# Optimization experiments

Hardware: AMD Instinct MI355X
Metric: run time of the kernel (lower is better)

## Reference

```python
import jax, jax.numpy as jnp
import numpy as np

EPS = 1e-12  # F.normalize default eps

def _l2norm(x, axis):
    n = jnp.sqrt(jnp.sum(x * x, axis=axis, keepdims=True))
    return x / jnp.maximum(n, EPS)

def setup_inputs() -> dict:
    key = jax.random.key(0)
    ks = jax.random.split(key, 6)
    N, C, K, B, OUT = 200000, 256, 64, 8, 1024
    alpha = 100.0
    feat = jax.random.normal(ks[0], (N, C), dtype=jnp.float32)
    batch_ids = jax.random.randint(ks[1], (N,), 0, B, dtype=jnp.int32)
    centroids = jax.random.uniform(ks[2], (K, C), dtype=jnp.float32)
    # _init_params: conv weight = 2*alpha*centroids, bias = -alpha*||centroid||_2
    conv_w = 2.0 * alpha * centroids
    conv_b = -alpha * jnp.sqrt(jnp.sum(centroids * centroids, axis=1))
    fc_w = jax.random.normal(ks[3], (OUT, K * C), dtype=jnp.float32) * (1.0 / np.sqrt(K * C))
    fc_b = jax.random.normal(ks[4], (OUT,), dtype=jnp.float32) * 0.01
    return {"feat": feat, "batch_ids": batch_ids, "centroids": centroids,
            "conv_w": conv_w, "conv_b": conv_b, "fc_w": fc_w, "fc_b": fc_b,
            "batch_size": B}

def reference(feat, batch_ids, centroids, conv_w, conv_b, fc_w, fc_b, batch_size):
    B = int(batch_size)
    K, C = centroids.shape
    # descriptor-wise L2 normalization (normalize_input=True)
    x = _l2norm(feat, axis=1)                       # [N, C]
    # 1x1 conv == linear: soft assignment logits per point
    logits = x @ conv_w.T + conv_b                  # [N, K]
    soft = jax.nn.softmax(logits, axis=1)           # [N, K]
    # Per-batch aggregation (replaces the python loop):
    # vlad[b,k,:] = sum_{p in b} soft[p,k] * x[p,:] - (sum_{p in b} soft[p,k]) * centroids[k,:]
    onehot = jax.nn.one_hot(batch_ids, B, dtype=x.dtype)          # [N, B]
    A = jnp.einsum('nb,nk,nc->bkc', onehot, soft, x)              # [B, K, C]
    S = jax.ops.segment_sum(soft, batch_ids, num_segments=B)      # [B, K]
    vlad = A - S[:, :, None] * centroids[None, :, :]              # [B, K, C]
    vlad = _l2norm(vlad, axis=2)                                  # intra-normalization over C
    v = vlad.reshape(B, K * C)
    out = v @ fc_w.T + fc_b                                       # [B, 1024]
    return _l2norm(out, axis=1)
```

## Files before the change

kernel.cpp:

```cpp
#include <hip/hip_runtime.h>
#include <hip/hip_bf16.h>

typedef __attribute__((ext_vector_type(8))) short bf16x8;
typedef __attribute__((ext_vector_type(4))) float f32x4;

#define PCAP 768

__device__ __forceinline__ void async_copy16(const void* g, void* l)
{
    __builtin_amdgcn_global_load_lds(
        (const __attribute__((address_space(1))) unsigned int*)g,
        (__attribute__((address_space(3))) unsigned int*)l, 16, 0, 0);
}

__global__ void p0_wsplit(const float* __restrict__ convw,
                          short* __restrict__ whi, short* __restrict__ wlo)
{
    int e = blockIdx.x * 256 + threadIdx.x;
    if (e >= 2048) return;
    int lane = e & 63;
    int kstep = (e >> 6) & 7;
    int nt = e >> 9;
    int cluster = nt * 16 + (lane & 15);
    int ch0 = kstep * 32 + (lane >> 4) * 8;
    const float* src = convw + cluster * 256 + ch0;
    #pragma unroll
    for (int j = 0; j < 8; ++j) {
        float x = src[j];
        unsigned u = __float_as_uint(x);
        unsigned uh = u & 0xffff0000u;
        float r = x - __uint_as_float(uh);
        whi[e * 8 + j] = (short)(u >> 16);
        wlo[e * 8 + j] = (short)(__float_as_uint(r) >> 16);
    }
}

__global__ __launch_bounds__(256, 2) void p1_mfma(
    const float* __restrict__ feat, const int* __restrict__ bids,
    const short* __restrict__ whi, const short* __restrict__ wlo,
    const float* __restrict__ convb,
    float* __restrict__ soft, float* __restrict__ invn, int* __restrict__ cnts, int N)
{
    __shared__ short whL[2048 * 8];
    __shared__ short wlL[2048 * 8];
    __shared__ int cnt[8];
    const int t = threadIdx.x;
    if (t < 8) cnt[t] = 0;
    const int w = t >> 6, lane = t & 63;
    const int m = lane & 15, quad = lane >> 4;
    const int p0 = blockIdx.x * 64;
    const int gp = p0 + w * 16 + m;
    const bool valid = gp < N;

    #pragma unroll
    for (int pass = 0; pass < 8; ++pass) {
        async_copy16((const bf16x8*)whi + pass * 256 + t,
                     (char*)whL + (size_t)(pass * 256 + w * 64) * 16);
        async_copy16((const bf16x8*)wlo + pass * 256 + t,
                     (char*)wlL + (size_t)(pass * 256 + w * 64) * 16);
    }

    const float* frow = valid ? (feat + (size_t)gp * 256 + quad * 8) : feat;
    float4 xv[16];
    #pragma unroll
    for (int ks = 0; ks < 8; ++ks) {
        xv[2 * ks]     = *(const float4*)(frow + ks * 32);
        xv[2 * ks + 1] = *(const float4*)(frow + ks * 32 + 4);
    }

    __syncthreads();

    f32x4 acc[4];
    #pragma unroll
    for (int nt = 0; nt < 4; ++nt) acc[nt] = (f32x4){0.f, 0.f, 0.f, 0.f};
    float ssq = 0.f;

    #pragma unroll
    for (int ks = 0; ks < 8; ++ks) {
        float x[8] = {xv[2 * ks].x, xv[2 * ks].y, xv[2 * ks].z, xv[2 * ks].w,
                      xv[2 * ks + 1].x, xv[2 * ks + 1].y, xv[2 * ks + 1].z, xv[2 * ks + 1].w};
        bf16x8 ahi, alo;
        #pragma unroll
        for (int j = 0; j < 8; ++j) {
            unsigned u = __float_as_uint(x[j]);
            float r = x[j] - __uint_as_float(u & 0xffff0000u);
            ahi[j] = (short)(u >> 16);
            alo[j] = (short)(__float_as_uint(r) >> 16);
            ssq += x[j] * x[j];
        }
        #pragma unroll
        for (int nt = 0; nt < 4; ++nt) {
            bf16x8 bh = *(const bf16x8*)&whL[(size_t)((nt * 8 + ks) * 64 + lane) * 8];
            bf16x8 bl = *(const bf16x8*)&wlL[(size_t)((nt * 8 + ks) * 64 + lane) * 8];
            acc[nt] = __builtin_amdgcn_mfma_f32_16x16x32_bf16(ahi, bh, acc[nt], 0, 0, 0);
            acc[nt] = __builtin_amdgcn_mfma_f32_16x16x32_bf16(ahi, bl, acc[nt], 0, 0, 0);
            acc[nt] = __builtin_amdgcn_mfma_f32_16x16x32_bf16(alo, bh, acc[nt], 0, 0, 0);
        }
    }

    ssq += __shfl_xor(ssq, 16);
    ssq += __shfl_xor(ssq, 32);

    float bias[4];
    #pragma unroll
    for (int nt = 0; nt < 4; ++nt) bias[nt] = convb[nt * 16 + m];

    #pragma unroll
    for (int r = 0; r < 4; ++r) {
        int pl = quad * 4 + r;
        int gpt = p0 + w * 16 + pl;
        float sq = __shfl(ssq, pl);
        float inv = rsqrtf(fmaxf(sq, 1e-24f));
        float v[4];
        #pragma unroll
        for (int nt = 0; nt < 4; ++nt) v[nt] = acc[nt][r] * inv + bias[nt];
        float mx = fmaxf(fmaxf(v[0], v[1]), fmaxf(v[2], v[3]));
        #pragma unroll
        for (int off = 8; off >= 1; off >>= 1) mx = fmaxf(mx, __shfl_xor(mx, off));
        float e[4];
        float s = 0.f;
        #pragma unroll
        for (int nt = 0; nt < 4; ++nt) { e[nt] = __expf(v[nt] - mx); s += e[nt]; }
        #pragma unroll
        for (int off = 8; off >= 1; off >>= 1) s += __shfl_xor(s, off);
        float rs = 1.0f / s;
        if (gpt < N) {
            #pragma unroll
            for (int nt = 0; nt < 4; ++nt)
                soft[(size_t)gpt * 64 + nt * 16 + m] = e[nt] * rs;
            if (m == 0) {
                invn[gpt] = inv;
                atomicAdd(&cnt[bids[gpt]], 1);
            }
        }
    }
    __syncthreads();
    if (t < 8) atomicAdd(&cnts[t], cnt[t]);
}

__global__ void p2_offsets(const int* __restrict__ cnts, int* __restrict__ offs, int* __restrict__ cur)
{
    if (threadIdx.x == 0) {
        int acc = 0;
        for (int b = 0; b < 8; ++b) { offs[b] = acc; cur[b] = acc; acc += cnts[b]; }
        offs[8] = acc;
    }
}

__global__ __launch_bounds__(256) void p2_scatter(
    const int* __restrict__ bids, int* __restrict__ cur, int* __restrict__ perm, int N)
{
    __shared__ int lcnt[8], lbase[8];
    const int t = threadIdx.x;
    if (t < 8) lcnt[t] = 0;
    __syncthreads();
    int p = blockIdx.x * 256 + t;
    int b = 0, my = 0;
    bool ok = p < N;
    if (ok) { b = bids[p]; my = atomicAdd(&lcnt[b], 1); }
    __syncthreads();
    if (t < 8) lbase[t] = atomicAdd(&cur[t], lcnt[t]);
    __syncthreads();
    if (ok) perm[lbase[b] + my] = p;
}

__global__ __launch_bounds__(256, 2) void p3_mfma(
    const float* __restrict__ feat, const float* __restrict__ soft,
    const float* __restrict__ invn, const int* __restrict__ perm,
    const int* __restrict__ offs, float* __restrict__ partial,
    float* __restrict__ S, int split)
{
    __shared__ short xsT_hi[256 * 32];
    __shared__ short xsT_lo[256 * 32];
    __shared__ short sT_hi[64 * 32];
    __shared__ short sT_lo[64 * 32];
    __shared__ int   pidxL[PCAP];
    __shared__ float invL[PCAP];

    const int b  = blockIdx.x / split;
    const int sp = blockIdx.x % split;
    const int start = offs[b], end = offs[b + 1];
    const int len = end - start;
    const int chunk = (len + split - 1) / split;
    const int s0 = start + sp * chunk;
    int myLen = end - s0;
    myLen = max(0, min(myLen, chunk));
    myLen = min(myLen, PCAP);

    const int t = threadIdx.x;
    const int w = t >> 6, lane = t & 63;
    const int m = lane & 15, quad = lane >> 4;

    for (int i = t; i < myLen; i += 256) pidxL[i] = perm[s0 + i];
    __syncthreads();
    for (int i = t; i < myLen; i += 256) invL[i] = invn[pidxL[i]];
    __syncthreads();

    f32x4 acc[16];
    #pragma unroll
    for (int ct = 0; ct < 16; ++ct) acc[ct] = (f32x4){0.f, 0.f, 0.f, 0.f};
    float sacc = 0.f;

    const int nch = (myLen + 31) >> 5;

    int   pids[8];
    float pinv[8];
    float xv[4][8];
    float sv[8];

    auto FETCH = [&](int q) {
        const int p0 = q * 32;
        #pragma unroll
        for (int j = 0; j < 8; ++j) {
            int pl = p0 + w * 8 + j;
            bool ok = pl < myLen;
            pids[j] = ok ? pidxL[pl] : -1;
            pinv[j] = ok ? invL[pl] : 0.f;
        }
        #pragma unroll
        for (int cg = 0; cg < 4; ++cg) {
            int c = cg * 64 + lane;
            #pragma unroll
            for (int j = 0; j < 8; ++j)
                xv[cg][j] = (pids[j] >= 0) ? feat[(size_t)pids[j] * 256 + c] : 0.f;
        }
        #pragma unroll
        for (int j = 0; j < 8; ++j)
            sv[j] = (pids[j] >= 0) ? soft[(size_t)pids[j] * 64 + lane] : 0.f;
    };

    if (nch > 0) FETCH(0);

    for (int q = 0; q < nch; ++q) {
        __syncthreads();
        #pragma unroll
        for (int cg = 0; cg < 4; ++cg) {
            int c = cg * 64 + lane;
            bf16x8 vh, vl;
            #pragma unroll
            for (int j = 0; j < 8; ++j) {
                float v = xv[cg][j] * pinv[j];
                unsigned u = __float_as_uint(v);
                float r = v - __uint_as_float(u & 0xffff0000u);
                vh[j] = (short)(u >> 16);
                vl[j] = (short)(__float_as_uint(r) >> 16);
            }
            int slot = (w ^ (c & 3)) * 8;
            *(bf16x8*)&xsT_hi[c * 32 + slot] = vh;
            *(bf16x8*)&xsT_lo[c * 32 + slot] = vl;
        }
        {
            bf16x8 vh, vl;
            #pragma unroll
            for (int j = 0; j < 8; ++j) {
                float v = sv[j];
                sacc += v;
                unsigned u = __float_as_uint(v);
                float r = v - __uint_as_float(u & 0xffff0000u);
                vh[j] = (short)(u >> 16);
                vl[j] = (short)(__float_as_uint(r) >> 16);
            }
            int slot = (w ^ (lane & 3)) * 8;
            *(bf16x8*)&sT_hi[lane * 32 + slot] = vh;
            *(bf16x8*)&sT_lo[lane * 32 + slot] = vl;
        }
        if (q + 1 < nch) FETCH(q + 1);
        __syncthreads();
        {
            const int arow = w * 16 + m;
            const int aslot = (quad ^ (m & 3)) * 8;
            bf16x8 ah = *(const bf16x8*)&sT_hi[arow * 32 + aslot];
            bf16x8 al = *(const bf16x8*)&sT_lo[arow * 32 + aslot];
            const int bslot = (quad ^ (m & 3)) * 8;
            #pragma unroll
            for (int ct = 0; ct < 16; ++ct) {
                const int brow = ct * 16 + m;
                bf16x8 bh = *(const bf16x8*)&xsT_hi[brow * 32 + bslot];
                bf16x8 bl = *(const bf16x8*)&xsT_lo[brow * 32 + bslot];
                acc[ct] = __builtin_amdgcn_mfma_f32_16x16x32_bf16(ah, bh, acc[ct], 0, 0, 0);
                acc[ct] = __builtin_amdgcn_mfma_f32_16x16x32_bf16(ah, bl, acc[ct], 0, 0, 0);
                acc[ct] = __builtin_amdgcn_mfma_f32_16x16x32_bf16(al, bh, acc[ct], 0, 0, 0);
            }
        }
    }

    float* dst = partial + (size_t)(b * split + sp) * 64 * 256;
    #pragma unroll
    for (int ct = 0; ct < 16; ++ct) {
        #pragma unroll
        for (int r = 0; r < 4; ++r) {
            int k = w * 16 + quad * 4 + r;
            dst[k * 256 + ct * 16 + m] = acc[ct][r];
        }
    }
    atomicAdd(S + b * 64 + lane, sacc);
}

__global__ __launch_bounds__(256) void p4a_vlad(
    const float* __restrict__ partial, const float* __restrict__ S,
    const float* __restrict__ cents, float* __restrict__ v, int split)
{
    const int b = blockIdx.x >> 6, k = blockIdx.x & 63;
    const int t = threadIdx.x;
    float sum = 0.f;
    const float* base = partial + ((size_t)(b * split) * 64 + k) * 256 + t;
    for (int sp = 0; sp < split; ++sp)
        sum += base[(size_t)sp * 64 * 256];
    float val = sum - S[b * 64 + k] * cents[k * 256 + t];
    float sq = val * val;
    #pragma unroll
    for (int off = 32; off >= 1; off >>= 1) sq += __shfl_xor(sq, off);
    __shared__ float wsum[4];
    if ((t & 63) == 0) wsum[t >> 6] = sq;
    __syncthreads();
    float tot = wsum[0] + wsum[1] + wsum[2] + wsum[3];
    float r = 1.0f / fmaxf(sqrtf(tot), 1e-12f);
    v[b * 16384 + k * 256 + t] = val * r;
}

__global__ __launch_bounds__(256) void p4b_fc(
    const float* __restrict__ v, const float* __restrict__ fcw,
    const float* __restrict__ fcb, float* __restrict__ pre)
{
    const int t = threadIdx.x;
    const int o0 = blockIdx.x * 4;
    float acc[4][8] = {};
    for (int it = 0; it < 64; ++it) {
        int i = it * 256 + t;
        float wv[4];
        #pragma unroll
        for (int oo = 0; oo < 4; ++oo) wv[oo] = fcw[(size_t)(o0 + oo) * 16384 + i];
        #pragma unroll
        for (int b = 0; b < 8; ++b) {
            float vv = v[b * 16384 + i];
            #pragma unroll
            for (int oo = 0; oo < 4; ++oo) acc[oo][b] += wv[oo] * vv;
        }
    }
    __shared__ float red[32][4];
    #pragma unroll
    for (int oo = 0; oo < 4; ++oo)
        #pragma unroll
        for (int b = 0; b < 8; ++b) {
            float sv = acc[oo][b];
            #pragma unroll
            for (int off = 32; off >= 1; off >>= 1) sv += __shfl_xor(sv, off);
            if ((t & 63) == 0) red[oo * 8 + b][t >> 6] = sv;
        }
    __syncthreads();
    if (t < 32) {
        int oo = t >> 3, b = t & 7;
        float sv = red[t][0] + red[t][1] + red[t][2] + red[t][3];
        pre[b * 1024 + o0 + oo] = sv + fcb[o0 + oo];
    }
}

__global__ __launch_bounds__(256) void p5_norm(const float* __restrict__ pre, float* __restrict__ out)
{
    const int b = blockIdx.x, t = threadIdx.x;
    float vals[4];
    float sq = 0.f;
    #pragma unroll
    for (int i = 0; i < 4; ++i) {
        vals[i] = pre[b * 1024 + t + 256 * i];
        sq += vals[i] * vals[i];
    }
    #pragma unroll
    for (int off = 32; off >= 1; off >>= 1) sq += __shfl_xor(sq, off);
    __shared__ float wsum[4];
    if ((t & 63) == 0) wsum[t >> 6] = sq;
    __syncthreads();
    float tot = wsum[0] + wsum[1] + wsum[2] + wsum[3];
    float r = 1.0f / fmaxf(sqrtf(tot), 1e-12f);
    #pragma unroll
    for (int i = 0; i < 4; ++i) out[b * 1024 + t + 256 * i] = vals[i] * r;
}

extern "C" void kernel_launch(void* const* d_in, const int* in_sizes, int n_in,
                              void* d_out, int out_size, void* d_ws, size_t ws_size,
                              hipStream_t stream)
{
    const float* feat  = (const float*)d_in[0];
    const int*   bids  = (const int*)d_in[1];
    const float* cents = (const float*)d_in[2];
    const float* convw = (const float*)d_in[3];
    const float* convb = (const float*)d_in[4];
    const float* fcw   = (const float*)d_in[5];
    const float* fcb   = (const float*)d_in[6];
    float* out = (float*)d_out;

    const int N = in_sizes[0] / 256;

    const size_t base_floats = 16384
                             + (size_t)N * 64  + N
                             + 512  + 8 * 16384  + 8192 ;
    const size_t base_ints = (size_t)N + 8 + 9 + 8;
    int split = 96;
    while (split > 16) {
        size_t tot = (base_floats + (size_t)split * 8 * 16384) * 4 + base_ints * 4;
        if (tot <= ws_size) break;
        split -= 16;
    }

    short* whi = (short*)d_ws;
    short* wlo = whi + 16384;
    float* soft = (float*)(wlo + 16384);
    float* invn = soft + (size_t)N * 64;
    float* partial = invn + N;
    float* S    = partial + (size_t)split * 8 * 16384;
    float* v    = S + 512;
    float* pre  = v + 8 * 16384;
    int* perm = (int*)(pre + 8192);
    int* cnts = perm + N;
    int* offs = cnts + 8;
    int* cur  = offs + 9;

    hipMemsetAsync(S, 0, 512 * sizeof(float), stream);
    hipMemsetAsync(cnts, 0, 8 * sizeof(int), stream);

    p0_wsplit<<<8, 256, 0, stream>>>(convw, whi, wlo);
    p1_mfma<<<(N + 63) / 64, 256, 0, stream>>>(feat, bids, whi, wlo, convb, soft, invn, cnts, N);
    p2_offsets<<<1, 64, 0, stream>>>(cnts, offs, cur);
    p2_scatter<<<(N + 255) / 256, 256, 0, stream>>>(bids, cur, perm, N);
    p3_mfma<<<8 * split, 256, 0, stream>>>(feat, soft, invn, perm, offs, partial, S, split);
    p4a_vlad<<<512, 256, 0, stream>>>(partial, S, cents, v, split);
    p4b_fc<<<256, 256, 0, stream>>>(v, fcw, fcb, pre);
    p5_norm<<<8, 256, 0, stream>>>(pre, out);
}
```

Before: 481.0 us.

## Fuse soft-assignment logits and softmax into the per-batch aggregation kernel

Removes the separate soft-assignment kernel. The aggregation kernel now recomputes each point's L2 norm, its 64 logits via split-bf16 MFMA and the softmax for every 32-point chunk it has gathered. This drops the full-size soft and invn intermediates, their global write and read-back, and one full pass over feat. A small kernel now only counts points per batch, and S is reduced through shared memory before the atomics. In exchange the aggregation loop gets extra MFMAs, shuffles and barriers, and it reloads feature rows straight from global memory for the logit GEMM, hoping they are still cached.

```diff
diff --git a/kernel.cpp b/kernel.cpp
--- a/kernel.cpp
+++ b/kernel.cpp
@@ -5,13 +5,6 @@
 typedef __attribute__((ext_vector_type(4))) float f32x4;
 
 #define PCAP 768
-
-__device__ __forceinline__ void async_copy16(const void* g, void* l)
-{
-    __builtin_amdgcn_global_load_lds(
-        (const __attribute__((address_space(1))) unsigned int*)g,
-        (__attribute__((address_space(3))) unsigned int*)l, 16, 0, 0);
-}
 
 __global__ void p0_wsplit(const float* __restrict__ convw,
                           short* __restrict__ whi, short* __restrict__ wlo)
@@ -35,107 +28,17 @@
     }
 }
 
-__global__ __launch_bounds__(256, 2) void p1_mfma(
-    const float* __restrict__ feat, const int* __restrict__ bids,
-    const short* __restrict__ whi, const short* __restrict__ wlo,
-    const float* __restrict__ convb,
-    float* __restrict__ soft, float* __restrict__ invn, int* __restrict__ cnts, int N)
-{
-    __shared__ short whL[2048 * 8];
-    __shared__ short wlL[2048 * 8];
-    __shared__ int cnt[8];
+__global__ __launch_bounds__(256) void p2a_count(
+    const int* __restrict__ bids, int* __restrict__ cnts, int N)
+{
+    __shared__ int lcnt[8];
     const int t = threadIdx.x;
-    if (t < 8) cnt[t] = 0;
-    const int w = t >> 6, lane = t & 63;
-    const int m = lane & 15, quad = lane >> 4;
-    const int p0 = blockIdx.x * 64;
-    const int gp = p0 + w * 16 + m;
-    const bool valid = gp < N;
-
-    #pragma unroll
-    for (int pass = 0; pass < 8; ++pass) {
-        async_copy16((const bf16x8*)whi + pass * 256 + t,
-                     (char*)whL + (size_t)(pass * 256 + w * 64) * 16);
-        async_copy16((const bf16x8*)wlo + pass * 256 + t,
-                     (char*)wlL + (size_t)(pass * 256 + w * 64) * 16);
-    }
-
-    const float* frow = valid ? (feat + (size_t)gp * 256 + quad * 8) : feat;
-    float4 xv[16];
-    #pragma unroll
-    for (int ks = 0; ks < 8; ++ks) {
-        xv[2 * ks]     = *(const float4*)(frow + ks * 32);
-        xv[2 * ks + 1] = *(const float4*)(frow + ks * 32 + 4);
-    }
-
-    __syncthreads();
-
-    f32x4 acc[4];
-    #pragma unroll
-    for (int nt = 0; nt < 4; ++nt) acc[nt] = (f32x4){0.f, 0.f, 0.f, 0.f};
-    float ssq = 0.f;
-
-    #pragma unroll
-    for (int ks = 0; ks < 8; ++ks) {
-        float x[8] = {xv[2 * ks].x, xv[2 * ks].y, xv[2 * ks].z, xv[2 * ks].w,
-                      xv[2 * ks + 1].x, xv[2 * ks + 1].y, xv[2 * ks + 1].z, xv[2 * ks + 1].w};
-        bf16x8 ahi, alo;
-        #pragma unroll
-        for (int j = 0; j < 8; ++j) {
-            unsigned u = __float_as_uint(x[j]);
-            float r = x[j] - __uint_as_float(u & 0xffff0000u);
-            ahi[j] = (short)(u >> 16);
-            alo[j] = (short)(__float_as_uint(r) >> 16);
-            ssq += x[j] * x[j];
-        }
-        #pragma unroll
-        for (int nt = 0; nt < 4; ++nt) {
-            bf16x8 bh = *(const bf16x8*)&whL[(size_t)((nt * 8 + ks) * 64 + lane) * 8];
-            bf16x8 bl = *(const bf16x8*)&wlL[(size_t)((nt * 8 + ks) * 64 + lane) * 8];
-            acc[nt] = __builtin_amdgcn_mfma_f32_16x16x32_bf16(ahi, bh, acc[nt], 0, 0, 0);
-            acc[nt] = __builtin_amdgcn_mfma_f32_16x16x32_bf16(ahi, bl, acc[nt], 0, 0, 0);
-            acc[nt] = __builtin_amdgcn_mfma_f32_16x16x32_bf16(alo, bh, acc[nt], 0, 0, 0);
-        }
-    }
-
-    ssq += __shfl_xor(ssq, 16);
-    ssq += __shfl_xor(ssq, 32);
-
-    float bias[4];
-    #pragma unroll
-    for (int nt = 0; nt < 4; ++nt) bias[nt] = convb[nt * 16 + m];
-
-    #pragma unroll
-    for (int r = 0; r < 4; ++r) {
-        int pl = quad * 4 + r;
-        int gpt = p0 + w * 16 + pl;
-        float sq = __shfl(ssq, pl);
-        float inv = rsqrtf(fmaxf(sq, 1e-24f));
-        float v[4];
-        #pragma unroll
-        for (int nt = 0; nt < 4; ++nt) v[nt] = acc[nt][r] * inv + bias[nt];
-        float mx = fmaxf(fmaxf(v[0], v[1]), fmaxf(v[2], v[3]));
-        #pragma unroll
-        for (int off = 8; off >= 1; off >>= 1) mx = fmaxf(mx, __shfl_xor(mx, off));
-        float e[4];
-        float s = 0.f;
-        #pragma unroll
-        for (int nt = 0; nt < 4; ++nt) { e[nt] = __expf(v[nt] - mx); s += e[nt]; }
-        #pragma unroll
-        for (int off = 8; off >= 1; off >>= 1) s += __shfl_xor(s, off);
-        float rs = 1.0f / s;
-        if (gpt < N) {
-            #pragma unroll
-            for (int nt = 0; nt < 4; ++nt)
-                soft[(size_t)gpt * 64 + nt * 16 + m] = e[nt] * rs;
-            if (m == 0) {
-                invn[gpt] = inv;
-                atomicAdd(&cnt[bids[gpt]], 1);
-            }
-        }
-    }
-    __syncthreads();
-    if (t < 8) atomicAdd(&cnts[t], cnt[t]);
+    if (t < 8) lcnt[t] = 0;
+    __syncthreads();
+    int p = blockIdx.x * 256 + t;
+    if (p < N) atomicAdd(&lcnt[bids[p]], 1);
+    __syncthreads();
+    if (t < 8) atomicAdd(&cnts[t], lcnt[t]);
 }
 
 __global__ void p2_offsets(const int* __restrict__ cnts, int* __restrict__ offs, int* __restrict__ cur)
@@ -164,18 +67,19 @@
     if (ok) perm[lbase[b] + my] = p;
 }
 
-__global__ __launch_bounds__(256, 2) void p3_mfma(
-    const float* __restrict__ feat, const float* __restrict__ soft,
-    const float* __restrict__ invn, const int* __restrict__ perm,
-    const int* __restrict__ offs, float* __restrict__ partial,
-    float* __restrict__ S, int split)
+__global__ __launch_bounds__(256, 2) void p3_fused(
+    const float* __restrict__ feat, const short* __restrict__ whi,
+    const short* __restrict__ wlo, const float* __restrict__ convb,
+    const int* __restrict__ perm, const int* __restrict__ offs,
+    float* __restrict__ partial, float* __restrict__ S, int split)
 {
     __shared__ short xsT_hi[256 * 32];
     __shared__ short xsT_lo[256 * 32];
     __shared__ short sT_hi[64 * 32];
     __shared__ short sT_lo[64 * 32];
+    __shared__ float logitsL[32 * 68];
+    __shared__ float invL32[32];
     __shared__ int   pidxL[PCAP];
-    __shared__ float invL[PCAP];
 
     const int b  = blockIdx.x / split;
     const int sp = blockIdx.x % split;
@@ -191,32 +95,28 @@
     const int w = t >> 6, lane = t & 63;
     const int m = lane & 15, quad = lane >> 4;
 
-    for (int i = t; i < myLen; i += 256) pidxL[i] = perm[s0 + i];
-    __syncthreads();
-    for (int i = t; i < myLen; i += 256) invL[i] = invn[pidxL[i]];
+    for (int i = t; i < PCAP; i += 256) pidxL[i] = (i < myLen) ? perm[s0 + i] : -1;
     __syncthreads();
 
     f32x4 acc[16];
     #pragma unroll
     for (int ct = 0; ct < 16; ++ct) acc[ct] = (f32x4){0.f, 0.f, 0.f, 0.f};
-    float sacc = 0.f;
+    float sacc[8];
+    #pragma unroll
+    for (int u = 0; u < 8; ++u) sacc[u] = 0.f;
+    float biask[8];
+    #pragma unroll
+    for (int u = 0; u < 8; ++u) biask[u] = convb[(t & 7) + 8 * u];
 
     const int nch = (myLen + 31) >> 5;
+    const bf16x8* WH = (const bf16x8*)whi;
+    const bf16x8* WL = (const bf16x8*)wlo;
 
     int   pids[8];
-    float pinv[8];
     float xv[4][8];
-    float sv[8];
-
     auto FETCH = [&](int q) {
-        const int p0 = q * 32;
-        #pragma unroll
-        for (int j = 0; j < 8; ++j) {
-            int pl = p0 + w * 8 + j;
-            bool ok = pl < myLen;
-            pids[j] = ok ? pidxL[pl] : -1;
-            pinv[j] = ok ? invL[pl] : 0.f;
-        }
+        #pragma unroll
+        for (int j = 0; j < 8; ++j) pids[j] = pidxL[q * 32 + w * 8 + j];
         #pragma unroll
         for (int cg = 0; cg < 4; ++cg) {
             int c = cg * 64 + lane;
@@ -224,22 +124,31 @@
             for (int j = 0; j < 8; ++j)
                 xv[cg][j] = (pids[j] >= 0) ? feat[(size_t)pids[j] * 256 + c] : 0.f;
         }
-        #pragma unroll
-        for (int j = 0; j < 8; ++j)
-            sv[j] = (pids[j] >= 0) ? soft[(size_t)pids[j] * 64 + lane] : 0.f;
     };
-
     if (nch > 0) FETCH(0);
 
     for (int q = 0; q < nch; ++q) {
         __syncthreads();
+        float inv[8];
+        #pragma unroll
+        for (int j = 0; j < 8; ++j) {
+            float ss = xv[0][j]*xv[0][j] + xv[1][j]*xv[1][j]
+                     + xv[2][j]*xv[2][j] + xv[3][j]*xv[3][j];
+            #pragma unroll
+            for (int off = 1; off < 64; off <<= 1) ss += __shfl_xor(ss, off);
+            inv[j] = rsqrtf(fmaxf(ss, 1e-24f));
+        }
+        if (lane == 0) {
+            #pragma unroll
+            for (int j = 0; j < 8; ++j) invL32[w * 8 + j] = inv[j];
+        }
         #pragma unroll
         for (int cg = 0; cg < 4; ++cg) {
             int c = cg * 64 + lane;
             bf16x8 vh, vl;
             #pragma unroll
             for (int j = 0; j < 8; ++j) {
-                float v = xv[cg][j] * pinv[j];
+                float v = xv[cg][j] * inv[j];
                 unsigned u = __float_as_uint(v);
                 float r = v - __uint_as_float(u & 0xffff0000u);
                 vh[j] = (short)(u >> 16);
@@ -249,22 +158,80 @@
             *(bf16x8*)&xsT_hi[c * 32 + slot] = vh;
             *(bf16x8*)&xsT_lo[c * 32 + slot] = vl;
         }
+        const int ptile = w >> 1;
+        const int kt0 = (w & 1) * 2;
+        const int apid = pidxL[q * 32 + ptile * 16 + m];
+        const float* abase = feat + (size_t)(apid >= 0 ? apid : 0) * 256 + quad * 8;
+        f32x4 acc2[2];
+        acc2[0] = (f32x4){0.f, 0.f, 0.f, 0.f};
+        acc2[1] = (f32x4){0.f, 0.f, 0.f, 0.f};
+        #pragma unroll
+        for (int cs = 0; cs < 8; ++cs) {
+            float4 a0 = *(const float4*)(abase + cs * 32);
+            float4 a1 = *(const float4*)(abase + cs * 32 + 4);
+            bf16x8 wh0 = WH[((kt0 + 0) * 8 + cs) * 64 + lane];
+            bf16x8 wl0 = WL[((kt0 + 0) * 8 + cs) * 64 + lane];
+            bf16x8 wh1 = WH[((kt0 + 1) * 8 + cs) * 64 + lane];
+            bf16x8 wl1 = WL[((kt0 + 1) * 8 + cs) * 64 + lane];
+            float xa[8] = {a0.x, a0.y, a0.z, a0.w, a1.x, a1.y, a1.z, a1.w};
+            if (apid < 0) {
+                #pragma unroll
+                for (int j = 0; j < 8; ++j) xa[j] = 0.f;
+            }
+            bf16x8 ahi, alo;
+            #pragma unroll
+            for (int j = 0; j < 8; ++j) {
+                unsigned u = __float_as_uint(xa[j]);
+                float r = xa[j] - __uint_as_float(u & 0xffff0000u);
+                ahi[j] = (short)(u >> 16);
+                alo[j] = (short)(__float_as_uint(r) >> 16);
+            }
+            acc2[0] = __builtin_amdgcn_mfma_f32_16x16x32_bf16(ahi, wh0, acc2[0], 0, 0, 0);
+            acc2[0] = __builtin_amdgcn_mfma_f32_16x16x32_bf16(ahi, wl0, acc2[0], 0, 0, 0);
+            acc2[0] = __builtin_amdgcn_mfma_f32_16x16x32_bf16(alo, wh0, acc2[0], 0, 0, 0);
+            acc2[1] = __builtin_amdgcn_mfma_f32_16x16x32_bf16(ahi, wh1, acc2[1], 0, 0, 0);
+            acc2[1] = __builtin_amdgcn_mfma_f32_16x16x32_bf16(ahi, wl1, acc2[1], 0, 0, 0);
+            acc2[1] = __builtin_amdgcn_mfma_f32_16x16x32_bf16(alo, wh1, acc2[1], 0, 0, 0);
+        }
+        if (q + 1 < nch) FETCH(q + 1);
+        #pragma unroll
+        for (int kt = 0; kt < 2; ++kt)
+            #pragma unroll
+            for (int r = 0; r < 4; ++r)
+                logitsL[(ptile * 16 + quad * 4 + r) * 68 + (kt0 + kt) * 16 + m] = acc2[kt][r];
+        __syncthreads();
         {
-            bf16x8 vh, vl;
-            #pragma unroll
-            for (int j = 0; j < 8; ++j) {
-                float v = sv[j];
-                sacc += v;
-                unsigned u = __float_as_uint(v);
-                float r = v - __uint_as_float(u & 0xffff0000u);
-                vh[j] = (short)(u >> 16);
-                vl[j] = (short)(__float_as_uint(r) >> 16);
+            const int p = t >> 3, s = t & 7;
+            const bool alive = (q * 32 + p) < myLen;
+            float iv = invL32[p];
+            float lg[8];
+            #pragma unroll
+            for (int u = 0; u < 8; ++u)
+                lg[u] = logitsL[p * 68 + s + 8 * u] * iv + biask[u];
+            float mx = lg[0];
+            #pragma unroll
+            for (int u = 1; u < 8; ++u) mx = fmaxf(mx, lg[u]);
+            #pragma unroll
+            for (int off = 1; off <= 4; off <<= 1) mx = fmaxf(mx, __shfl_xor(mx, off));
+            float e[8];
+            float ssum = 0.f;
+            #pragma unroll
+            for (int u = 0; u < 8; ++u) { e[u] = __expf(lg[u] - mx); ssum += e[u]; }
+            #pragma unroll
+            for (int off = 1; off <= 4; off <<= 1) ssum += __shfl_xor(ssum, off);
+            float rs = 1.0f / ssum;
+            #pragma unroll
+            for (int u = 0; u < 8; ++u) {
+                float sv = alive ? e[u] * rs : 0.f;
+                sacc[u] += sv;
+                int k = s + 8 * u;
+                unsigned uu = __float_as_uint(sv);
+                float rr = sv - __uint_as_float(uu & 0xffff0000u);
+                int idx = k * 32 + (((p >> 3) ^ (k & 3)) * 8) + (p & 7);
+                sT_hi[idx] = (short)(uu >> 16);
+                sT_lo[idx] = (short)(__float_as_uint(rr) >> 16);
             }
-            int slot = (w ^ (lane & 3)) * 8;
-            *(bf16x8*)&sT_hi[lane * 32 + slot] = vh;
-            *(bf16x8*)&sT_lo[lane * 32 + slot] = vl;
-        }
-        if (q + 1 < nch) FETCH(q + 1);
+        }
         __syncthreads();
         {
             const int arow = w * 16 + m;
@@ -284,6 +251,24 @@
         }
     }
 
+    #pragma unroll
+    for (int u = 0; u < 8; ++u) {
+        sacc[u] += __shfl_xor(sacc[u], 8);
+        sacc[u] += __shfl_xor(sacc[u], 16);
+        sacc[u] += __shfl_xor(sacc[u], 32);
+    }
+    __syncthreads();
+    float* swred = logitsL;
+    if (lane < 8) {
+        #pragma unroll
+        for (int u = 0; u < 8; ++u) swred[w * 64 + lane + 8 * u] = sacc[u];
+    }
+    __syncthreads();
+    if (t < 64) {
+        float sv = swred[t] + swred[64 + t] + swred[128 + t] + swred[192 + t];
+        atomicAdd(S + b * 64 + t, sv);
+    }
+
     float* dst = partial + (size_t)(b * split + sp) * 64 * 256;
     #pragma unroll
     for (int ct = 0; ct < 16; ++ct) {
@@ -293,7 +278,6 @@
             dst[k * 256 + ct * 16 + m] = acc[ct][r];
         }
     }
-    atomicAdd(S + b * 64 + lane, sacc);
 }
 
 __global__ __launch_bounds__(256) void p4a_vlad(
@@ -392,7 +376,6 @@
     const int N = in_sizes[0] / 256;
 
     const size_t base_floats = 16384
-                             + (size_t)N * 64  + N
                              + 512  + 8 * 16384  + 8192 ;
     const size_t base_ints = (size_t)N + 8 + 9 + 8;
     int split = 96;
@@ -404,9 +387,7 @@
 
     short* whi = (short*)d_ws;
     short* wlo = whi + 16384;
-    float* soft = (float*)(wlo + 16384);
-    float* invn = soft + (size_t)N * 64;
-    float* partial = invn + N;
+    float* partial = (float*)(wlo + 16384);
     float* S    = partial + (size_t)split * 8 * 16384;
     float* v    = S + 512;
     float* pre  = v + 8 * 16384;
@@ -419,10 +400,10 @@
     hipMemsetAsync(cnts, 0, 8 * sizeof(int), stream);
 
     p0_wsplit<<<8, 256, 0, stream>>>(convw, whi, wlo);
-    p1_mfma<<<(N + 63) / 64, 256, 0, stream>>>(feat, bids, whi, wlo, convb, soft, invn, cnts, N);
+    p2a_count<<<(N + 255) / 256, 256, 0, stream>>>(bids, cnts, N);
     p2_offsets<<<1, 64, 0, stream>>>(cnts, offs, cur);
     p2_scatter<<<(N + 255) / 256, 256, 0, stream>>>(bids, cur, perm, N);
-    p3_mfma<<<8 * split, 256, 0, stream>>>(feat, soft, invn, perm, offs, partial, S, split);
+    p3_fused<<<8 * split, 256, 0, stream>>>(feat, whi, wlo, convb, perm, offs, partial, S, split);
     p4a_vlad<<<512, 256, 0, stream>>>(partial, S, cents, v, split);
     p4b_fc<<<256, 256, 0, stream>>>(v, fcw, fcb, pre);
     p5_norm<<<8, 256, 0, stream>>>(pre, out);
```

New measurement: 597.4 us. 1.24x slower.

## Make soft-assignment kernel persistent to amortize weight staging; move batch counting out

Applied to the files above, without the earlier changes.

The soft-assignment MFMA kernel becomes a persistent grid of 512 blocks of 512 threads, where each wave loops over 16-point tiles. The split conv weights are now staged into LDS once per block instead of once per 64 points. The per-batch counting atomics are moved out into a separate lightweight count kernel. This cuts the repeated 64KB LDS weight load per small block, at the cost of an extra kernel launch and an extra pass over batch_ids. The feature loads are no longer overlapped with the weight copy.

```diff
diff --git a/kernel.cpp b/kernel.cpp
--- a/kernel.cpp
+++ b/kernel.cpp
@@ -35,107 +35,118 @@
     }
 }
 
-__global__ __launch_bounds__(256, 2) void p1_mfma(
-    const float* __restrict__ feat, const int* __restrict__ bids,
+__global__ __launch_bounds__(512, 4) void p1_mfma(
+    const float* __restrict__ feat,
     const short* __restrict__ whi, const short* __restrict__ wlo,
     const float* __restrict__ convb,
-    float* __restrict__ soft, float* __restrict__ invn, int* __restrict__ cnts, int N)
+    float* __restrict__ soft, float* __restrict__ invn, int N)
 {
     __shared__ short whL[2048 * 8];
     __shared__ short wlL[2048 * 8];
-    __shared__ int cnt[8];
-    const int t = threadIdx.x;
-    if (t < 8) cnt[t] = 0;
+    const int t = threadIdx.x;
     const int w = t >> 6, lane = t & 63;
     const int m = lane & 15, quad = lane >> 4;
-    const int p0 = blockIdx.x * 64;
-    const int gp = p0 + w * 16 + m;
-    const bool valid = gp < N;
-
-    #pragma unroll
-    for (int pass = 0; pass < 8; ++pass) {
-        async_copy16((const bf16x8*)whi + pass * 256 + t,
-                     (char*)whL + (size_t)(pass * 256 + w * 64) * 16);
-        async_copy16((const bf16x8*)wlo + pass * 256 + t,
-                     (char*)wlL + (size_t)(pass * 256 + w * 64) * 16);
-    }
-
-    const float* frow = valid ? (feat + (size_t)gp * 256 + quad * 8) : feat;
-    float4 xv[16];
-    #pragma unroll
-    for (int ks = 0; ks < 8; ++ks) {
-        xv[2 * ks]     = *(const float4*)(frow + ks * 32);
-        xv[2 * ks + 1] = *(const float4*)(frow + ks * 32 + 4);
-    }
-
-    __syncthreads();
-
-    f32x4 acc[4];
-    #pragma unroll
-    for (int nt = 0; nt < 4; ++nt) acc[nt] = (f32x4){0.f, 0.f, 0.f, 0.f};
-    float ssq = 0.f;
-
-    #pragma unroll
-    for (int ks = 0; ks < 8; ++ks) {
-        float x[8] = {xv[2 * ks].x, xv[2 * ks].y, xv[2 * ks].z, xv[2 * ks].w,
-                      xv[2 * ks + 1].x, xv[2 * ks + 1].y, xv[2 * ks + 1].z, xv[2 * ks + 1].w};
-        bf16x8 ahi, alo;
-        #pragma unroll
-        for (int j = 0; j < 8; ++j) {
-            unsigned u = __float_as_uint(x[j]);
-            float r = x[j] - __uint_as_float(u & 0xffff0000u);
-            ahi[j] = (short)(u >> 16);
-            alo[j] = (short)(__float_as_uint(r) >> 16);
-            ssq += x[j] * x[j];
-        }
-        #pragma unroll
-        for (int nt = 0; nt < 4; ++nt) {
-            bf16x8 bh = *(const bf16x8*)&whL[(size_t)((nt * 8 + ks) * 64 + lane) * 8];
-            bf16x8 bl = *(const bf16x8*)&wlL[(size_t)((nt * 8 + ks) * 64 + lane) * 8];
-            acc[nt] = __builtin_amdgcn_mfma_f32_16x16x32_bf16(ahi, bh, acc[nt], 0, 0, 0);
-            acc[nt] = __builtin_amdgcn_mfma_f32_16x16x32_bf16(ahi, bl, acc[nt], 0, 0, 0);
-            acc[nt] = __builtin_amdgcn_mfma_f32_16x16x32_bf16(alo, bh, acc[nt], 0, 0, 0);
-        }
-    }
-
-    ssq += __shfl_xor(ssq, 16);
-    ssq += __shfl_xor(ssq, 32);
+
+    #pragma unroll
+    for (int pass = 0; pass < 4; ++pass) {
+        async_copy16((const bf16x8*)whi + pass * 512 + t,
+                     (char*)whL + (size_t)(pass * 512 + w * 64) * 16);
+        async_copy16((const bf16x8*)wlo + pass * 512 + t,
+                     (char*)wlL + (size_t)(pass * 512 + w * 64) * 16);
+    }
+    __syncthreads();
 
     float bias[4];
     #pragma unroll
     for (int nt = 0; nt < 4; ++nt) bias[nt] = convb[nt * 16 + m];
 
-    #pragma unroll
-    for (int r = 0; r < 4; ++r) {
-        int pl = quad * 4 + r;
-        int gpt = p0 + w * 16 + pl;
-        float sq = __shfl(ssq, pl);
-        float inv = rsqrtf(fmaxf(sq, 1e-24f));
-        float v[4];
-        #pragma unroll
-        for (int nt = 0; nt < 4; ++nt) v[nt] = acc[nt][r] * inv + bias[nt];
-        float mx = fmaxf(fmaxf(v[0], v[1]), fmaxf(v[2], v[3]));
-        #pragma unroll
-        for (int off = 8; off >= 1; off >>= 1) mx = fmaxf(mx, __shfl_xor(mx, off));
-        float e[4];
-        float s = 0.f;
-        #pragma unroll
-        for (int nt = 0; nt < 4; ++nt) { e[nt] = __expf(v[nt] - mx); s += e[nt]; }
-        #pragma unroll
-        for (int off = 8; off >= 1; off >>= 1) s += __shfl_xor(s, off);
-        float rs = 1.0f / s;
-        if (gpt < N) {
-            #pragma unroll
-            for (int nt = 0; nt < 4; ++nt)
-                soft[(size_t)gpt * 64 + nt * 16 + m] = e[nt] * rs;
-            if (m == 0) {
-                invn[gpt] = inv;
-                atomicAdd(&cnt[bids[gpt]], 1);
-            }
-        }
-    }
-    __syncthreads();
-    if (t < 8) atomicAdd(&cnts[t], cnt[t]);
+    const int gw = blockIdx.x * 8 + w;
+    const int nwaves = gridDim.x * 8;
+    const int ntiles = (N + 15) >> 4;
+
+    for (int tile = gw; tile < ntiles; tile += nwaves) {
+        const int gp = tile * 16 + m;
+        const bool valid = gp < N;
+        const float* frow = valid ? (feat + (size_t)gp * 256 + quad * 8) : feat;
+
+        float4 xv[16];
+        #pragma unroll
+        for (int ks = 0; ks < 8; ++ks) {
+            xv[2 * ks]     = *(const float4*)(frow + ks * 32);
+            xv[2 * ks + 1] = *(const float4*)(frow + ks * 32 + 4);
+        }
+
+        f32x4 acc[4];
+        #pragma unroll
+        for (int nt = 0; nt < 4; ++nt) acc[nt] = (f32x4){0.f, 0.f, 0.f, 0.f};
+        float ssq = 0.f;
+
+        #pragma unroll
+        for (int ks = 0; ks < 8; ++ks) {
+            float x[8] = {xv[2 * ks].x, xv[2 * ks].y, xv[2 * ks].z, xv[2 * ks].w,
+                          xv[2 * ks + 1].x, xv[2 * ks + 1].y, xv[2 * ks + 1].z, xv[2 * ks + 1].w};
+            bf16x8 ahi, alo;
+            #pragma unroll
+            for (int j = 0; j < 8; ++j) {
+                unsigned u = __float_as_uint(x[j]);
+                float r = x[j] - __uint_as_float(u & 0xffff0000u);
+                ahi[j] = (short)(u >> 16);
+                alo[j] = (short)(__float_as_uint(r) >> 16);
+                ssq += x[j] * x[j];
+            }
+            #pragma unroll
+            for (int nt = 0; nt < 4; ++nt) {
+                bf16x8 bh = *(const bf16x8*)&whL[(size_t)((nt * 8 + ks) * 64 + lane) * 8];
+                bf16x8 bl = *(const bf16x8*)&wlL[(size_t)((nt * 8 + ks) * 64 + lane) * 8];
+                acc[nt] = __builtin_amdgcn_mfma_f32_16x16x32_bf16(ahi, bh, acc[nt], 0, 0, 0);
+                acc[nt] = __builtin_amdgcn_mfma_f32_16x16x32_bf16(ahi, bl, acc[nt], 0, 0, 0);
+                acc[nt] = __builtin_amdgcn_mfma_f32_16x16x32_bf16(alo, bh, acc[nt], 0, 0, 0);
+            }
+        }
+
+        ssq += __shfl_xor(ssq, 16);
+        ssq += __shfl_xor(ssq, 32);
+
+        #pragma unroll
+        for (int r = 0; r < 4; ++r) {
+            int pl = quad * 4 + r;
+            int gpt = tile * 16 + pl;
+            float sq = __shfl(ssq, pl);
+            float inv = rsqrtf(fmaxf(sq, 1e-24f));
+            float v[4];
+            #pragma unroll
+            for (int nt = 0; nt < 4; ++nt) v[nt] = acc[nt][r] * inv + bias[nt];
+            float mx = fmaxf(fmaxf(v[0], v[1]), fmaxf(v[2], v[3]));
+            #pragma unroll
+            for (int off = 8; off >= 1; off >>= 1) mx = fmaxf(mx, __shfl_xor(mx, off));
+            float e[4];
+            float s = 0.f;
+            #pragma unroll
+            for (int nt = 0; nt < 4; ++nt) { e[nt] = __expf(v[nt] - mx); s += e[nt]; }
+            #pragma unroll
+            for (int off = 8; off >= 1; off >>= 1) s += __shfl_xor(s, off);
+            float rs = 1.0f / s;
+            if (gpt < N) {
+                #pragma unroll
+                for (int nt = 0; nt < 4; ++nt)
+                    soft[(size_t)gpt * 64 + nt * 16 + m] = e[nt] * rs;
+                if (m == 0) invn[gpt] = inv;
+            }
+        }
+    }
+}
+
+__global__ __launch_bounds__(256) void p2a_count(
+    const int* __restrict__ bids, int* __restrict__ cnts, int N)
+{
+    __shared__ int lcnt[8];
+    const int t = threadIdx.x;
+    if (t < 8) lcnt[t] = 0;
+    __syncthreads();
+    int p = blockIdx.x * 256 + t;
+    if (p < N) atomicAdd(&lcnt[bids[p]], 1);
+    __syncthreads();
+    if (t < 8) atomicAdd(&cnts[t], lcnt[t]);
 }
 
 __global__ void p2_offsets(const int* __restrict__ cnts, int* __restrict__ offs, int* __restrict__ cur)
@@ -419,7 +430,8 @@
     hipMemsetAsync(cnts, 0, 8 * sizeof(int), stream);
 
     p0_wsplit<<<8, 256, 0, stream>>>(convw, whi, wlo);
-    p1_mfma<<<(N + 63) / 64, 256, 0, stream>>>(feat, bids, whi, wlo, convb, soft, invn, cnts, N);
+    p1_mfma<<<512, 512, 0, stream>>>(feat, whi, wlo, convb, soft, invn, N);
+    p2a_count<<<(N + 255) / 256, 256, 0, stream>>>(bids, cnts, N);
     p2_offsets<<<1, 64, 0, stream>>>(cnts, offs, cur);
     p2_scatter<<<(N + 255) / 256, 256, 0, stream>>>(bids, cur, perm, N);
     p3_mfma<<<8 * split, 256, 0, stream>>>(feat, soft, invn, perm, offs, partial, S, split);
```

New measurement: 700.4 us. 45.6% more time.

## Make p1 persistent with double-buffered register prefetch of feature tiles

Applied to the files above, without the earlier changes.

The soft-assignment kernel now runs as a persistent grid of 640 blocks that loop over 64-point tiles in a grid stride. Each block loads the conv weight split into LDS only once. Feature rows for the next tile are prefetched into a second register buffer while the current tile runs its MFMA and softmax work, with sched barriers keeping the loads ahead. This removes the per-block weight reload and overlaps global-load latency with compute, at the cost of higher register pressure, which may lower occupancy or cause spills.

```diff
diff --git a/kernel.cpp b/kernel.cpp
--- a/kernel.cpp
+++ b/kernel.cpp
@@ -48,9 +48,6 @@
     if (t < 8) cnt[t] = 0;
     const int w = t >> 6, lane = t & 63;
     const int m = lane & 15, quad = lane >> 4;
-    const int p0 = blockIdx.x * 64;
-    const int gp = p0 + w * 16 + m;
-    const bool valid = gp < N;
 
     #pragma unroll
     for (int pass = 0; pass < 8; ++pass) {
@@ -59,81 +56,101 @@
         async_copy16((const bf16x8*)wlo + pass * 256 + t,
                      (char*)wlL + (size_t)(pass * 256 + w * 64) * 16);
     }
-
-    const float* frow = valid ? (feat + (size_t)gp * 256 + quad * 8) : feat;
-    float4 xv[16];
-    #pragma unroll
-    for (int ks = 0; ks < 8; ++ks) {
-        xv[2 * ks]     = *(const float4*)(frow + ks * 32);
-        xv[2 * ks + 1] = *(const float4*)(frow + ks * 32 + 4);
-    }
-
-    __syncthreads();
-
-    f32x4 acc[4];
-    #pragma unroll
-    for (int nt = 0; nt < 4; ++nt) acc[nt] = (f32x4){0.f, 0.f, 0.f, 0.f};
-    float ssq = 0.f;
-
-    #pragma unroll
-    for (int ks = 0; ks < 8; ++ks) {
-        float x[8] = {xv[2 * ks].x, xv[2 * ks].y, xv[2 * ks].z, xv[2 * ks].w,
-                      xv[2 * ks + 1].x, xv[2 * ks + 1].y, xv[2 * ks + 1].z, xv[2 * ks + 1].w};
-        bf16x8 ahi, alo;
-        #pragma unroll
-        for (int j = 0; j < 8; ++j) {
-            unsigned u = __float_as_uint(x[j]);
-            float r = x[j] - __uint_as_float(u & 0xffff0000u);
-            ahi[j] = (short)(u >> 16);
-            alo[j] = (short)(__float_as_uint(r) >> 16);
-            ssq += x[j] * x[j];
-        }
-        #pragma unroll
-        for (int nt = 0; nt < 4; ++nt) {
-            bf16x8 bh = *(const bf16x8*)&whL[(size_t)((nt * 8 + ks) * 64 + lane) * 8];
-            bf16x8 bl = *(const bf16x8*)&wlL[(size_t)((nt * 8 + ks) * 64 + lane) * 8];
-            acc[nt] = __builtin_amdgcn_mfma_f32_16x16x32_bf16(ahi, bh, acc[nt], 0, 0, 0);
-            acc[nt] = __builtin_amdgcn_mfma_f32_16x16x32_bf16(ahi, bl, acc[nt], 0, 0, 0);
-            acc[nt] = __builtin_amdgcn_mfma_f32_16x16x32_bf16(alo, bh, acc[nt], 0, 0, 0);
-        }
-    }
-
-    ssq += __shfl_xor(ssq, 16);
-    ssq += __shfl_xor(ssq, 32);
+    __syncthreads();
 
     float bias[4];
     #pragma unroll
     for (int nt = 0; nt < 4; ++nt) bias[nt] = convb[nt * 16 + m];
 
-    #pragma unroll
-    for (int r = 0; r < 4; ++r) {
-        int pl = quad * 4 + r;
-        int gpt = p0 + w * 16 + pl;
-        float sq = __shfl(ssq, pl);
-        float inv = rsqrtf(fmaxf(sq, 1e-24f));
-        float v[4];
-        #pragma unroll
-        for (int nt = 0; nt < 4; ++nt) v[nt] = acc[nt][r] * inv + bias[nt];
-        float mx = fmaxf(fmaxf(v[0], v[1]), fmaxf(v[2], v[3]));
-        #pragma unroll
-        for (int off = 8; off >= 1; off >>= 1) mx = fmaxf(mx, __shfl_xor(mx, off));
-        float e[4];
-        float s = 0.f;
-        #pragma unroll
-        for (int nt = 0; nt < 4; ++nt) { e[nt] = __expf(v[nt] - mx); s += e[nt]; }
-        #pragma unroll
-        for (int off = 8; off >= 1; off >>= 1) s += __shfl_xor(s, off);
-        float rs = 1.0f / s;
-        if (gpt < N) {
-            #pragma unroll
-            for (int nt = 0; nt < 4; ++nt)
-                soft[(size_t)gpt * 64 + nt * 16 + m] = e[nt] * rs;
-            if (m == 0) {
-                invn[gpt] = inv;
-                atomicAdd(&cnt[bids[gpt]], 1);
-            }
-        }
-    }
+    const int NT = (N + 63) >> 6;
+    const int G = gridDim.x;
+
+    float4 xvA[16], xvB[16];
+
+    auto LOAD = [&](float4 (&xv)[16], int tile) {
+        int gp = tile * 64 + w * 16 + m;
+        const float* frow = (gp < N) ? (feat + (size_t)gp * 256 + quad * 8) : feat;
+        #pragma unroll
+        for (int ks = 0; ks < 8; ++ks) {
+            xv[2 * ks]     = *(const float4*)(frow + ks * 32);
+            xv[2 * ks + 1] = *(const float4*)(frow + ks * 32 + 4);
+        }
+    };
+
+    auto COMPUTE = [&](const float4 (&xv)[16], int tile) {
+        f32x4 acc[4];
+        #pragma unroll
+        for (int nt = 0; nt < 4; ++nt) acc[nt] = (f32x4){0.f, 0.f, 0.f, 0.f};
+        float ssq = 0.f;
+        #pragma unroll
+        for (int ks = 0; ks < 8; ++ks) {
+            float x[8] = {xv[2 * ks].x, xv[2 * ks].y, xv[2 * ks].z, xv[2 * ks].w,
+                          xv[2 * ks + 1].x, xv[2 * ks + 1].y, xv[2 * ks + 1].z, xv[2 * ks + 1].w};
+            bf16x8 ahi, alo;
+            #pragma unroll
+            for (int j = 0; j < 8; ++j) {
+                unsigned u = __float_as_uint(x[j]);
+                float r = x[j] - __uint_as_float(u & 0xffff0000u);
+                ahi[j] = (short)(u >> 16);
+                alo[j] = (short)(__float_as_uint(r) >> 16);
+                ssq += x[j] * x[j];
+            }
+            #pragma unroll
+            for (int nt = 0; nt < 4; ++nt) {
+                bf16x8 bh = *(const bf16x8*)&whL[(size_t)((nt * 8 + ks) * 64 + lane) * 8];
+                bf16x8 bl = *(const bf16x8*)&wlL[(size_t)((nt * 8 + ks) * 64 + lane) * 8];
+                acc[nt] = __builtin_amdgcn_mfma_f32_16x16x32_bf16(ahi, bh, acc[nt], 0, 0, 0);
+                acc[nt] = __builtin_amdgcn_mfma_f32_16x16x32_bf16(ahi, bl, acc[nt], 0, 0, 0);
+                acc[nt] = __builtin_amdgcn_mfma_f32_16x16x32_bf16(alo, bh, acc[nt], 0, 0, 0);
+            }
+        }
+        ssq += __shfl_xor(ssq, 16);
+        ssq += __shfl_xor(ssq, 32);
+        #pragma unroll
+        for (int r = 0; r < 4; ++r) {
+            int pl = quad * 4 + r;
+            int gpt = tile * 64 + w * 16 + pl;
+            float sq = __shfl(ssq, pl);
+            float inv = rsqrtf(fmaxf(sq, 1e-24f));
+            float v[4];
+            #pragma unroll
+            for (int nt = 0; nt < 4; ++nt) v[nt] = acc[nt][r] * inv + bias[nt];
+            float mx = fmaxf(fmaxf(v[0], v[1]), fmaxf(v[2], v[3]));
+            #pragma unroll
+            for (int off = 8; off >= 1; off >>= 1) mx = fmaxf(mx, __shfl_xor(mx, off));
+            float e[4];
+            float s = 0.f;
+            #pragma unroll
+            for (int nt = 0; nt < 4; ++nt) { e[nt] = __expf(v[nt] - mx); s += e[nt]; }
+            #pragma unroll
+            for (int off = 8; off >= 1; off >>= 1) s += __shfl_xor(s, off);
+            float rs = 1.0f / s;
+            if (gpt < N) {
+                #pragma unroll
+                for (int nt = 0; nt < 4; ++nt)
+                    soft[(size_t)gpt * 64 + nt * 16 + m] = e[nt] * rs;
+                if (m == 0) {
+                    invn[gpt] = inv;
+                    atomicAdd(&cnt[bids[gpt]], 1);
+                }
+            }
+        }
+    };
+
+    int t0 = blockIdx.x;
+    if (t0 < NT) LOAD(xvA, t0);
+    while (t0 < NT) {
+        int t1 = t0 + G;
+        if (t1 < NT) LOAD(xvB, t1);
+        __builtin_amdgcn_sched_barrier(0);
+        COMPUTE(xvA, t0);
+        int t2 = t1 + G;
+        if (t2 < NT) LOAD(xvA, t2);
+        __builtin_amdgcn_sched_barrier(0);
+        if (t1 < NT) COMPUTE(xvB, t1);
+        t0 = t2;
+    }
+
     __syncthreads();
     if (t < 8) atomicAdd(&cnts[t], cnt[t]);
 }
@@ -419,7 +436,7 @@
     hipMemsetAsync(cnts, 0, 8 * sizeof(int), stream);
 
     p0_wsplit<<<8, 256, 0, stream>>>(convw, whi, wlo);
-    p1_mfma<<<(N + 63) / 64, 256, 0, stream>>>(feat, bids, whi, wlo, convb, soft, invn, cnts, N);
+    p1_mfma<<<640, 256, 0, stream>>>(feat, bids, whi, wlo, convb, soft, invn, cnts, N);
     p2_offsets<<<1, 64, 0, stream>>>(cnts, offs, cur);
     p2_scatter<<<(N + 255) / 256, 256, 0, stream>>>(bids, cur, perm, N);
     p3_mfma<<<8 * split, 256, 0, stream>>>(feat, soft, invn, perm, offs, partial, S, split);
```

Result: slower. 492.0 us (+2.3%).
